# Kernel tuning notes

Hardware: AMD Instinct MI355X
Metric: run time of the kernel (lower is better)

Reference implementation:

```python
import jax, jax.numpy as jnp
import numpy as np

SCALING = 128.0 / 64  # alpha / rank = 2.0
EPS = 1e-8


def setup_inputs() -> dict:
    key = jax.random.key(0)
    ks = jax.random.split(key, 5)
    B, S, D_IN, D_OUT, R = 2, 4096, 4096, 4096, 64
    x = jax.random.normal(ks[0], (B, S, D_IN), dtype=jnp.float32)
    base_output = jax.random.normal(ks[1], (B, S, D_OUT), dtype=jnp.float32)
    base_weight = jax.random.normal(ks[2], (D_OUT, D_IN), dtype=jnp.float32) * 0.02
    lora_A = jax.random.normal(ks[3], (R, D_IN), dtype=jnp.float32) * 0.02
    lora_B = jax.random.normal(ks[4], (D_OUT, R), dtype=jnp.float32) * 0.02
    magnitude = jnp.ones((D_OUT,), dtype=jnp.float32)
    return {"x": x, "base_output": base_output, "base_weight": base_weight,
            "lora_A": lora_A, "lora_B": lora_B, "magnitude": magnitude}


def reference(x, base_output, base_weight, lora_A, lora_B, magnitude):
    # LoRA path: x @ A^T @ B^T, scaled  (dropout p=0 -> identity)
    xa = jnp.einsum('bsd,rd->bsr', x, lora_A)          # [B,S,r]
    delta_v = jnp.einsum('bsr,or->bso', xa, lora_B) * SCALING  # [B,S,out]
    # Updated weight and its per-row L2 norm
    updated_weight = base_weight + (lora_B @ lora_A) * SCALING  # [out,in]
    updated_norm = jnp.sqrt(jnp.sum(updated_weight * updated_weight, axis=1))  # [out]
    mag_scale = magnitude / (updated_norm + EPS)  # [out]
    combined = base_output + delta_v
    return combined * mag_scale[None, None, :]
```

## Files before the change

kernel.cpp:

```cpp
#include <hip/hip_runtime.h>
#include <math.h>

typedef __bf16 bf16x8 __attribute__((ext_vector_type(8)));
typedef float f32x4 __attribute__((ext_vector_type(4)));

#define MFMA16(a, b, c) __builtin_amdgcn_mfma_f32_16x16x32_bf16(a, b, c, 0, 0, 0)

static constexpr int M_TOT = 8192;
static constexpr int DIN = 4096;
static constexpr int DOUT = 4096;
static constexpr int RNK = 64;

__device__ inline unsigned short f2bf(float f) {
    union { float f; unsigned u; } v; v.f = f;
    unsigned r = v.u + 0x7FFFu + ((v.u >> 16) & 1u);
    return (unsigned short)(r >> 16);
}

__global__ __launch_bounds__(256) void k_prep(const float* __restrict__ A,
                                              const float* __restrict__ B,
                                              unsigned short* __restrict__ Afrag,
                                              unsigned short* __restrict__ Atfrag,
                                              unsigned short* __restrict__ Bfrag) {
    int i = blockIdx.x * 256 + threadIdx.x;
    unsigned short ab = f2bf(A[i]);
    int n = i >> 12, k = i & 4095;
    Afrag[(((k >> 5) << 2) + (n >> 4)) * 512 +
          ((((k >> 3) & 3) << 4) + (n & 15)) * 8 + (k & 7)] = ab;
    Atfrag[(((k >> 4) << 1) + (n >> 5)) * 512 +
           ((((n >> 3) & 3) << 4) + (k & 15)) * 8 + (n & 7)] = ab;
    unsigned short bb = f2bf(B[i]);
    int o = i >> 6, r = i & 63;
    Bfrag[(((o >> 4) << 1) + (r >> 5)) * 512 +
          ((((r >> 3) & 3) << 4) + (o & 15)) * 8 + (r & 7)] = bb;
}

__global__ __launch_bounds__(256) void k1_xa(const float* __restrict__ x,
                                             const unsigned short* __restrict__ Afrag,
                                             float* __restrict__ pxa) {
    __shared__ __align__(16) char smem[16640];
    unsigned short (*stage)[520] = (unsigned short (*)[520])smem;
    float (*red)[1024] = (float (*)[1024])smem;
    int tid = threadIdx.x;
    int wid = tid >> 6, lane = tid & 63;
    int row = lane & 15, kq = lane >> 4;
    int lane8 = lane * 8;
    int mt = blockIdx.x & 511, kpart = blockIdx.x >> 9;
    int m0 = mt * 16;
    int sr = tid >> 4, sc = (tid & 15) * 4;

    const float* xp = x + (size_t)(m0 + sr) * DIN + kpart * 2048 + sc;

    f32x4 r[8];
    #pragma unroll
    for (int p = 0; p < 8; ++p) r[p] = *(const f32x4*)(xp + p * 64);

    f32x4 acc0 = {0.f, 0.f, 0.f, 0.f};
    f32x4 acc1 = acc0, acc2 = acc0, acc3 = acc0;

    for (int c = 0; c < 4; ++c) {
        __syncthreads();
        #pragma unroll
        for (int p = 0; p < 8; ++p) {
            ushort4 h;
            h.x = f2bf(r[p][0]); h.y = f2bf(r[p][1]);
            h.z = f2bf(r[p][2]); h.w = f2bf(r[p][3]);
            *(ushort4*)&stage[sr][p * 64 + sc] = h;
        }
        __syncthreads();
        if (c < 3) {
            const float* nx = xp + (c + 1) * 512;
            #pragma unroll
            for (int p = 0; p < 8; ++p) r[p] = *(const f32x4*)(nx + p * 64);
        }
        #pragma unroll
        for (int s = 0; s < 4; ++s) {
            bf16x8 af = *(const bf16x8*)&stage[row][wid * 128 + s * 32 + kq * 8];
            int ks = (kpart * 2048 + c * 512 + wid * 128 + s * 32) >> 5;
            const unsigned short* ap = Afrag + (size_t)(ks << 2) * 512 + lane8;
            acc0 = MFMA16(af, *(const bf16x8*)(ap), acc0);
            acc1 = MFMA16(af, *(const bf16x8*)(ap + 512), acc1);
            acc2 = MFMA16(af, *(const bf16x8*)(ap + 1024), acc2);
            acc3 = MFMA16(af, *(const bf16x8*)(ap + 1536), acc3);
        }
    }
    __syncthreads();

    int mb = kq * 4;
    #pragma unroll
    for (int rg = 0; rg < 4; ++rg) {
        red[wid][(mb + rg) * 64 + row]      = acc0[rg];
        red[wid][(mb + rg) * 64 + 16 + row] = acc1[rg];
        red[wid][(mb + rg) * 64 + 32 + row] = acc2[rg];
        red[wid][(mb + rg) * 64 + 48 + row] = acc3[rg];
    }
    __syncthreads();
    #pragma unroll
    for (int e = tid; e < 1024; e += 256) {
        float s = red[0][e] + red[1][e] + red[2][e] + red[3][e];
        pxa[(size_t)kpart * M_TOT * RNK + (size_t)(m0 + (e >> 6)) * RNK + (e & 63)] = s;
    }
}

__global__ __launch_bounds__(256) void k1_fin(const float* __restrict__ pxa,
                                              unsigned short* __restrict__ xafrag) {
    int tid = threadIdx.x;
    int mt = blockIdx.x;
    int e0 = tid * 4;
    size_t o = (size_t)(mt * 16 + (e0 >> 6)) * RNK + (e0 & 63);
    f32x4 s0 = *(const f32x4*)(pxa + o);
    f32x4 s1 = *(const f32x4*)(pxa + (size_t)M_TOT * RNK + o);
    int ml = e0 >> 6, r0 = e0 & 63;
    ushort4 h;
    h.x = f2bf(s0[0] + s1[0]);
    h.y = f2bf(s0[1] + s1[1]);
    h.z = f2bf(s0[2] + s1[2]);
    h.w = f2bf(s0[3] + s1[3]);
    *(ushort4*)&xafrag[((size_t)(mt * 2 + (r0 >> 5))) * 512 +
                       ((((r0 >> 3) & 3) << 4) + ml) * 8 + (r0 & 7)] = h;
}

__global__ __launch_bounds__(256) void k2_norm(const float* __restrict__ bw,
                                               const unsigned short* __restrict__ Bfrag,
                                               const unsigned short* __restrict__ Atfrag,
                                               float* __restrict__ pn) {
    __shared__ __align__(16) char smem[16896];
    float (*stagef)[260] = (float (*)[260])smem;
    float (*part)[16] = (float (*)[16])(smem + 16640);
    int tid = threadIdx.x;
    int wid = tid >> 6, lane = tid & 63;
    int row = lane & 15, kq = lane >> 4;
    int lane8 = lane * 8;
    int ot = blockIdx.x & 255, ipart = blockIdx.x >> 8;
    int o0 = ot * 16;
    int sr = tid >> 4, sc = (tid & 15) * 4;

    const float* bwp = bw + (size_t)(o0 + sr) * DIN + ipart * 1024 + sc;

    f32x4 q[4];
    #pragma unroll
    for (int p = 0; p < 4; ++p) q[p] = *(const f32x4*)(bwp + p * 64);

    bf16x8 b0 = *(const bf16x8*)(Bfrag + (size_t)(ot * 2) * 512 + lane8);
    bf16x8 b1 = *(const bf16x8*)(Bfrag + (size_t)(ot * 2 + 1) * 512 + lane8);

    f32x4 nacc = {0.f, 0.f, 0.f, 0.f};

    for (int c = 0; c < 4; ++c) {
        __syncthreads();
        #pragma unroll
        for (int p = 0; p < 4; ++p) *(f32x4*)&stagef[sr][p * 64 + sc] = q[p];
        __syncthreads();
        if (c < 3) {
            const float* nb = bwp + (c + 1) * 256;
            #pragma unroll
            for (int p = 0; p < 4; ++p) q[p] = *(const f32x4*)(nb + p * 64);
        }
        #pragma unroll
        for (int g = 0; g < 4; ++g) {
            int iloc = wid * 64 + g * 16;
            int it = (ipart * 1024 + c * 256 + iloc) >> 4;
            const unsigned short* atp = Atfrag + (size_t)(it * 2) * 512 + lane8;
            bf16x8 a0 = *(const bf16x8*)(atp);
            bf16x8 a1 = *(const bf16x8*)(atp + 512);
            f32x4 d = {0.f, 0.f, 0.f, 0.f};
            d = MFMA16(a0, b0, d);
            d = MFMA16(a1, b1, d);
            f32x4 wv = *(const f32x4*)&stagef[row][iloc + kq * 4];
            #pragma unroll
            for (int rg = 0; rg < 4; ++rg) {
                float w = wv[rg] + 2.0f * d[rg];
                nacc[rg] += w * w;
            }
        }
    }
    float ns = nacc[0] + nacc[1] + nacc[2] + nacc[3];
    ns += __shfl_xor(ns, 16, 64);
    ns += __shfl_xor(ns, 32, 64);
    if (kq == 0) part[wid][row] = ns;
    __syncthreads();
    if (tid < 16)
        pn[ipart * DOUT + o0 + tid] =
            part[0][tid] + part[1][tid] + part[2][tid] + part[3][tid];
}

__global__ __launch_bounds__(256) void k2b_scale(const float* __restrict__ pn,
                                                 const float* __restrict__ mag,
                                                 float* __restrict__ mscale) {
    int o = blockIdx.x * 256 + threadIdx.x;
    float n2 = 0.f;
    #pragma unroll
    for (int p = 0; p < 4; ++p) n2 += pn[p * DOUT + o];
    mscale[o] = mag[o] / (sqrtf(n2) + 1e-8f);
}

__global__ __launch_bounds__(256) void kB(const float* __restrict__ base,
                                          const unsigned short* __restrict__ xafrag,
                                          const unsigned short* __restrict__ Bfrag,
                                          const float* __restrict__ mscale,
                                          float* __restrict__ out) {
    __shared__ float dls[32][260];
    int tid = threadIdx.x;
    int wid = tid >> 6, lane = tid & 63;
    int row = lane & 15, kq = lane >> 4;
    int m0 = blockIdx.x * 32;
    int n0 = blockIdx.y * 256;
    int col = n0 + lane * 4;
    int lane8 = lane * 8;

    f32x4 bpre[2][4];
    #pragma unroll
    for (int h = 0; h < 2; ++h)
        #pragma unroll
        for (int r = 0; r < 4; ++r)
            bpre[h][r] = __builtin_nontemporal_load(
                (const f32x4*)(base + (size_t)(m0 + h * 16 + wid * 4 + r) * DOUT + col));
    f32x4 msv = *(const f32x4*)(mscale + col);

    bf16x8 xb0[2], xb1[2];
    #pragma unroll
    for (int h = 0; h < 2; ++h) {
        size_t mt = (size_t)(blockIdx.x * 2 + h);
        xb0[h] = *(const bf16x8*)(xafrag + (mt * 2) * 512 + lane8);
        xb1[h] = *(const bf16x8*)(xafrag + (mt * 2 + 1) * 512 + lane8);
    }

    #pragma unroll
    for (int nt = 0; nt < 4; ++nt) {
        size_t ntg = (size_t)((n0 + wid * 64 + nt * 16) >> 4);
        bf16x8 a0 = *(const bf16x8*)(Bfrag + (ntg * 2) * 512 + lane8);
        bf16x8 a1 = *(const bf16x8*)(Bfrag + (ntg * 2 + 1) * 512 + lane8);
        #pragma unroll
        for (int h = 0; h < 2; ++h) {
            f32x4 acc = {0.f, 0.f, 0.f, 0.f};
            acc = MFMA16(a0, xb0[h], acc);
            acc = MFMA16(a1, xb1[h], acc);
            *(f32x4*)&dls[h * 16 + row][wid * 64 + nt * 16 + kq * 4] = acc;
        }
    }
    __syncthreads();

    #pragma unroll
    for (int h = 0; h < 2; ++h)
        #pragma unroll
        for (int r = 0; r < 4; ++r) {
            int m = h * 16 + wid * 4 + r;
            f32x4 d = *(const f32x4*)&dls[m][lane * 4];
            size_t gidx = (size_t)(m0 + m) * DOUT + col;
            f32x4 o;
            #pragma unroll
            for (int j = 0; j < 4; ++j) o[j] = (bpre[h][r][j] + 2.0f * d[j]) * msv[j];
            __builtin_nontemporal_store(o, (f32x4*)(out + gidx));
        }
}

extern "C" void kernel_launch(void* const* d_in, const int* in_sizes, int n_in,
                              void* d_out, int out_size, void* d_ws, size_t ws_size,
                              hipStream_t stream) {
    const float* x    = (const float*)d_in[0];
    const float* base = (const float*)d_in[1];
    const float* bw   = (const float*)d_in[2];
    const float* lA   = (const float*)d_in[3];
    const float* lB   = (const float*)d_in[4];
    const float* mag  = (const float*)d_in[5];
    float* out = (float*)d_out;

    char* ws = (char*)d_ws;
    unsigned short* Afrag  = (unsigned short*)(ws);
    unsigned short* Atfrag = (unsigned short*)(ws + (512u << 10));
    unsigned short* Bfrag  = (unsigned short*)(ws + (1024u << 10));
    unsigned short* xafrag = (unsigned short*)(ws + (1536u << 10));
    float*          pxa    = (float*)(ws + (2560u << 10));
    float*          pn     = (float*)(ws + (6656u << 10));
    float*          msc    = (float*)(ws + (6720u << 10));

    hipLaunchKernelGGL(k_prep, dim3(1024), dim3(256), 0, stream, lA, lB, Afrag, Atfrag, Bfrag);
    hipLaunchKernelGGL(k1_xa, dim3(1024), dim3(256), 0, stream, x, Afrag, pxa);
    hipLaunchKernelGGL(k2_norm, dim3(1024), dim3(256), 0, stream, bw, Bfrag, Atfrag, pn);
    hipLaunchKernelGGL(k1_fin, dim3(512), dim3(256), 0, stream, pxa, xafrag);
    hipLaunchKernelGGL(k2b_scale, dim3(DOUT / 256), dim3(256), 0, stream, pn, mag, msc);
    hipLaunchKernelGGL(kB, dim3(M_TOT / 32, DOUT / 256), dim3(256), 0, stream,
                       base, xafrag, Bfrag, msc, out);
}
```

Measured before the change: 119.3 us.

## Double-buffer x and weight tiles via direct global-to-LDS loads with swizzle

Replaces the register-staged loads in the xA and norm kernels with direct global-to-LDS loads into two XOR-swizzled shared buffers. The A and A^T fragments for the next chunk are prefetched into registers while the current chunk is computed. In the xA kernel the fp32-to-bf16 conversion now happens after the LDS read instead of before the LDS write, so x is staged in LDS as fp32. This aims to overlap memory latency with MFMA work and cut register traffic, at the cost of doubled LDS use and more live registers, which may lower occupancy.

```diff
diff --git a/kernel.cpp b/kernel.cpp
--- a/kernel.cpp
+++ b/kernel.cpp
@@ -15,6 +15,12 @@
     union { float f; unsigned u; } v; v.f = f;
     unsigned r = v.u + 0x7FFFu + ((v.u >> 16) & 1u);
     return (unsigned short)(r >> 16);
+}
+
+__device__ inline void gload_lds16(const float* g, char* lds_base) {
+    __builtin_amdgcn_global_load_lds(
+        (const __attribute__((address_space(1))) void*)g,
+        (__attribute__((address_space(3))) void*)lds_base, 16, 0, 0);
 }
 
 __global__ __launch_bounds__(256) void k_prep(const float* __restrict__ A,
@@ -38,8 +44,9 @@
 __global__ __launch_bounds__(256) void k1_xa(const float* __restrict__ x,
                                              const unsigned short* __restrict__ Afrag,
                                              float* __restrict__ pxa) {
-    __shared__ __align__(16) char smem[16640];
-    unsigned short (*stage)[520] = (unsigned short (*)[520])smem;
+    __shared__ __align__(16) char smem[32768];
+    char* buf0 = smem;
+    char* buf1 = smem + 16384;
     float (*red)[1024] = (float (*)[1024])smem;
     int tid = threadIdx.x;
     int wid = tid >> 6, lane = tid & 63;
@@ -47,44 +54,63 @@
     int lane8 = lane * 8;
     int mt = blockIdx.x & 511, kpart = blockIdx.x >> 9;
     int m0 = mt * 16;
-    int sr = tid >> 4, sc = (tid & 15) * 4;
-
-    const float* xp = x + (size_t)(m0 + sr) * DIN + kpart * 2048 + sc;
-
-    f32x4 r[8];
-    #pragma unroll
-    for (int p = 0; p < 8; ++p) r[p] = *(const f32x4*)(xp + p * 64);
+    int swzr = (row & 7) << 4;
+    const float* xbase = x + (size_t)m0 * DIN + kpart * 2048;
 
     f32x4 acc0 = {0.f, 0.f, 0.f, 0.f};
     f32x4 acc1 = acc0, acc2 = acc0, acc3 = acc0;
-
-    for (int c = 0; c < 4; ++c) {
+    bf16x8 setA[8], setB[8];
+
+    auto STAGE = [&](char* buf, int c) {
+        #pragma unroll
+        for (int j = 0; j < 4; ++j) {
+            int r = wid * 4 + j;
+            int srcb = (lane * 16) ^ ((r & 7) << 4);
+            const float* g = xbase + (size_t)r * DIN + c * 256 + (srcb >> 2);
+            gload_lds16(g, buf + r * 1024);
+        }
+    };
+    auto AFRAG = [&](bf16x8* set, int c) {
+        #pragma unroll
+        for (int s = 0; s < 2; ++s) {
+            int ks = kpart * 64 + c * 8 + wid * 2 + s;
+            const unsigned short* ap = Afrag + (size_t)ks * 2048 + lane8;
+            set[s * 4 + 0] = *(const bf16x8*)(ap);
+            set[s * 4 + 1] = *(const bf16x8*)(ap + 512);
+            set[s * 4 + 2] = *(const bf16x8*)(ap + 1024);
+            set[s * 4 + 3] = *(const bf16x8*)(ap + 1536);
+        }
+    };
+    auto COMPUTE = [&](const char* buf, const bf16x8* set) {
+        #pragma unroll
+        for (int s = 0; s < 2; ++s) {
+            int kbyte = wid * 256 + s * 128 + kq * 32;
+            f32x4 xlo = *(const f32x4*)(buf + row * 1024 + ((kbyte) ^ swzr));
+            f32x4 xhi = *(const f32x4*)(buf + row * 1024 + ((kbyte + 16) ^ swzr));
+            bf16x8 af;
+            #pragma unroll
+            for (int j = 0; j < 4; ++j) {
+                af[j] = (__bf16)xlo[j];
+                af[j + 4] = (__bf16)xhi[j];
+            }
+            acc0 = MFMA16(af, set[s * 4 + 0], acc0);
+            acc1 = MFMA16(af, set[s * 4 + 1], acc1);
+            acc2 = MFMA16(af, set[s * 4 + 2], acc2);
+            acc3 = MFMA16(af, set[s * 4 + 3], acc3);
+        }
+    };
+
+    STAGE(buf0, 0); AFRAG(setA, 0);
+    __syncthreads();
+    #pragma unroll
+    for (int c = 0; c < 8; c += 2) {
+        if (c + 1 < 8) { STAGE(buf1, c + 1); AFRAG(setB, c + 1); }
+        COMPUTE(buf0, setA);
         __syncthreads();
-        #pragma unroll
-        for (int p = 0; p < 8; ++p) {
-            ushort4 h;
-            h.x = f2bf(r[p][0]); h.y = f2bf(r[p][1]);
-            h.z = f2bf(r[p][2]); h.w = f2bf(r[p][3]);
-            *(ushort4*)&stage[sr][p * 64 + sc] = h;
-        }
+        if (c + 2 < 8) { STAGE(buf0, c + 2); AFRAG(setA, c + 2); }
+        if (c + 1 < 8) COMPUTE(buf1, setB);
         __syncthreads();
-        if (c < 3) {
-            const float* nx = xp + (c + 1) * 512;
-            #pragma unroll
-            for (int p = 0; p < 8; ++p) r[p] = *(const f32x4*)(nx + p * 64);
-        }
-        #pragma unroll
-        for (int s = 0; s < 4; ++s) {
-            bf16x8 af = *(const bf16x8*)&stage[row][wid * 128 + s * 32 + kq * 8];
-            int ks = (kpart * 2048 + c * 512 + wid * 128 + s * 32) >> 5;
-            const unsigned short* ap = Afrag + (size_t)(ks << 2) * 512 + lane8;
-            acc0 = MFMA16(af, *(const bf16x8*)(ap), acc0);
-            acc1 = MFMA16(af, *(const bf16x8*)(ap + 512), acc1);
-            acc2 = MFMA16(af, *(const bf16x8*)(ap + 1024), acc2);
-            acc3 = MFMA16(af, *(const bf16x8*)(ap + 1536), acc3);
-        }
-    }
-    __syncthreads();
+    }
 
     int mb = kq * 4;
     #pragma unroll
@@ -124,56 +150,71 @@
                                                const unsigned short* __restrict__ Bfrag,
                                                const unsigned short* __restrict__ Atfrag,
                                                float* __restrict__ pn) {
-    __shared__ __align__(16) char smem[16896];
-    float (*stagef)[260] = (float (*)[260])smem;
-    float (*part)[16] = (float (*)[16])(smem + 16640);
+    __shared__ __align__(16) char smem[32768];
+    __shared__ float part[4][16];
+    char* buf0 = smem;
+    char* buf1 = smem + 16384;
     int tid = threadIdx.x;
     int wid = tid >> 6, lane = tid & 63;
     int row = lane & 15, kq = lane >> 4;
     int lane8 = lane * 8;
     int ot = blockIdx.x & 255, ipart = blockIdx.x >> 8;
     int o0 = ot * 16;
-    int sr = tid >> 4, sc = (tid & 15) * 4;
-
-    const float* bwp = bw + (size_t)(o0 + sr) * DIN + ipart * 1024 + sc;
-
-    f32x4 q[4];
-    #pragma unroll
-    for (int p = 0; p < 4; ++p) q[p] = *(const f32x4*)(bwp + p * 64);
+    int swzr = (row & 7) << 4;
+    const float* bwbase = bw + (size_t)o0 * DIN + ipart * 1024;
 
     bf16x8 b0 = *(const bf16x8*)(Bfrag + (size_t)(ot * 2) * 512 + lane8);
     bf16x8 b1 = *(const bf16x8*)(Bfrag + (size_t)(ot * 2 + 1) * 512 + lane8);
 
     f32x4 nacc = {0.f, 0.f, 0.f, 0.f};
-
-    for (int c = 0; c < 4; ++c) {
-        __syncthreads();
-        #pragma unroll
-        for (int p = 0; p < 4; ++p) *(f32x4*)&stagef[sr][p * 64 + sc] = q[p];
-        __syncthreads();
-        if (c < 3) {
-            const float* nb = bwp + (c + 1) * 256;
-            #pragma unroll
-            for (int p = 0; p < 4; ++p) q[p] = *(const f32x4*)(nb + p * 64);
-        }
+    bf16x8 setA[8], setB[8];
+
+    auto STAGE = [&](char* buf, int c) {
+        #pragma unroll
+        for (int j = 0; j < 4; ++j) {
+            int r = wid * 4 + j;
+            int srcb = (lane * 16) ^ ((r & 7) << 4);
+            const float* g = bwbase + (size_t)r * DIN + c * 256 + (srcb >> 2);
+            gload_lds16(g, buf + r * 1024);
+        }
+    };
+    auto ATFRAG = [&](bf16x8* set, int c) {
         #pragma unroll
         for (int g = 0; g < 4; ++g) {
-            int iloc = wid * 64 + g * 16;
-            int it = (ipart * 1024 + c * 256 + iloc) >> 4;
-            const unsigned short* atp = Atfrag + (size_t)(it * 2) * 512 + lane8;
-            bf16x8 a0 = *(const bf16x8*)(atp);
-            bf16x8 a1 = *(const bf16x8*)(atp + 512);
+            int it = ipart * 64 + c * 16 + wid * 4 + g;
+            const unsigned short* atp = Atfrag + (size_t)it * 1024 + lane8;
+            set[g * 2]     = *(const bf16x8*)(atp);
+            set[g * 2 + 1] = *(const bf16x8*)(atp + 512);
+        }
+    };
+    auto COMPUTE = [&](const char* buf, const bf16x8* set) {
+        #pragma unroll
+        for (int g = 0; g < 4; ++g) {
             f32x4 d = {0.f, 0.f, 0.f, 0.f};
-            d = MFMA16(a0, b0, d);
-            d = MFMA16(a1, b1, d);
-            f32x4 wv = *(const f32x4*)&stagef[row][iloc + kq * 4];
+            d = MFMA16(set[g * 2], b0, d);
+            d = MFMA16(set[g * 2 + 1], b1, d);
+            int ibyte = wid * 256 + g * 64 + kq * 16;
+            f32x4 wv = *(const f32x4*)(buf + row * 1024 + (ibyte ^ swzr));
             #pragma unroll
             for (int rg = 0; rg < 4; ++rg) {
                 float w = wv[rg] + 2.0f * d[rg];
                 nacc[rg] += w * w;
             }
         }
-    }
+    };
+
+    STAGE(buf0, 0); ATFRAG(setA, 0);
+    __syncthreads();
+    #pragma unroll
+    for (int c = 0; c < 4; c += 2) {
+        if (c + 1 < 4) { STAGE(buf1, c + 1); ATFRAG(setB, c + 1); }
+        COMPUTE(buf0, setA);
+        __syncthreads();
+        if (c + 2 < 4) { STAGE(buf0, c + 2); ATFRAG(setA, c + 2); }
+        if (c + 1 < 4) COMPUTE(buf1, setB);
+        __syncthreads();
+    }
+
     float ns = nacc[0] + nacc[1] + nacc[2] + nacc[3];
     ns += __shfl_xor(ns, 16, 64);
     ns += __shfl_xor(ns, 32, 64);
```

Measured after the change: 113.4 us. 1.05x faster.
